# Optimization experiments

Measured on AMD Instinct MI355X. Metric: run time of the kernel, lower is better.

The kernel has to match this reference:

```python
import jax, jax.numpy as jnp
import numpy as np

USER = 100000
ITEM = 50000
N = USER + ITEM
LATDIM = 64
IMG_DIM = 1024
E_ADJ = 3_000_000
E_IMG = 1_000_000
GNN_LAYERS = 2
RIS_LAMBDA = 1.0
EPS = 1e-12


def spmm(rows, cols, vals, x):
    # sparse [N,N] @ dense [N,D] via gather + segment-sum
    return jax.ops.segment_sum(vals[:, None] * x[cols], rows, num_segments=N)


def setup_inputs() -> dict:
    key = jax.random.key(0)
    ks = jax.random.split(key, 10)
    return {
        "adj_rows": jax.random.randint(ks[0], (E_ADJ,), 0, N, dtype=jnp.int32),
        "adj_cols": jax.random.randint(ks[1], (E_ADJ,), 0, N, dtype=jnp.int32),
        "adj_vals": jax.random.uniform(ks[2], (E_ADJ,), dtype=jnp.float32),
        "img_rows": jax.random.randint(ks[3], (E_IMG,), 0, N, dtype=jnp.int32),
        "img_cols": jax.random.randint(ks[4], (E_IMG,), 0, N, dtype=jnp.int32),
        "img_vals": jax.random.uniform(ks[5], (E_IMG,), dtype=jnp.float32),
        "image_embedding": jax.random.normal(ks[6], (ITEM, IMG_DIM), dtype=jnp.float32),
        "uEmbeds": jax.random.normal(ks[7], (USER, LATDIM), dtype=jnp.float32) * 0.01,
        "iEmbeds": jax.random.normal(ks[8], (ITEM, LATDIM), dtype=jnp.float32) * 0.01,
        "W_trans": jax.random.normal(ks[9], (IMG_DIM, LATDIM), dtype=jnp.float32) * (1.0 / np.sqrt(IMG_DIM)),
        "b_trans": jnp.zeros((LATDIM,), dtype=jnp.float32),
    }


def reference(adj_rows, adj_cols, adj_vals, img_rows, img_cols, img_vals,
              image_embedding, uEmbeds, iEmbeds, W_trans, b_trans):
    # trans == 1: Linear projection of image features
    image_feats = image_embedding @ W_trans + b_trans  # [ITEM, LATDIM]

    # image_adj @ concat(u, i)
    embeds_img_adj = spmm(img_rows, img_cols, img_vals, jnp.concatenate([uEmbeds, iEmbeds], axis=0))

    # F.normalize(image_feats) along dim=1 (L2, eps=1e-12)
    nrm = jnp.linalg.norm(image_feats, axis=1, keepdims=True)
    feats_n = image_feats / jnp.maximum(nrm, EPS)

    embeds_image = spmm(adj_rows, adj_cols, adj_vals, jnp.concatenate([uEmbeds, feats_n], axis=0))
    embeds_image_ = spmm(adj_rows, adj_cols, adj_vals,
                         jnp.concatenate([embeds_image[:USER], iEmbeds], axis=0))
    embeds_image = embeds_image + embeds_image_ + RIS_LAMBDA * embeds_img_adj

    # stacked GCN layers with sum over all layer outputs (including input)
    acc = embeds_image
    cur = embeds_image
    for _ in range(GNN_LAYERS):
        cur = spmm(adj_rows, adj_cols, adj_vals, cur)
        acc = acc + cur

    return acc[:USER], acc[USER:]
```

## Files before the change

kernel.cpp:

```cpp
#include <hip/hip_runtime.h>
#include <hip/hip_fp16.h>

#define USER_N 100000
#define ITEM_N 50000
#define NN (USER_N + ITEM_N)
#define D 64
#define IMGD 1024
#define LDP 68

#define BUCKET_BITS 10
#define BROWS (1 << BUCKET_BITS)
#define NBUCK ((NN + BROWS - 1) >> BUCKET_BITS)
#define CHUNK 4096

typedef _Float16 v4h __attribute__((ext_vector_type(4)));
typedef _Float16 v8h __attribute__((ext_vector_type(8)));
typedef float v4f __attribute__((ext_vector_type(4)));

__global__ __launch_bounds__(256) void wt_prep(
    const float* __restrict__ W, _Float16* __restrict__ Wt16)
{
    const int id = blockIdx.x * 256 + threadIdx.x;
    if (id >= D * IMGD) return;
    const int c = id >> 10;
    const int k = id & 1023;
    Wt16[id] = (_Float16)W[(size_t)k * D + c];
}

#define GAS2 68
__global__ __launch_bounds__(256) void gemm_mfma2(
    const float* __restrict__ A, const _Float16* __restrict__ Wt16,
    const float* __restrict__ b, float* __restrict__ C)
{
    __shared__ _Float16 Af[2][32][GAS2];
    const int t = threadIdx.x;
    const int w = t >> 6;
    const int lane = t & 63;
    const int l16 = lane & 15;
    const int g = lane >> 4;
    const int row0 = blockIdx.x * 32;
    const int wr = (w >> 1) * 16;
    const int wc = (w & 1) * 32;

    v4f acc[2] = {};

    const int lrow0 = t >> 4;
    const int lrow1 = lrow0 + 16;
    const int lk = (t & 15) * 4;
    const int ga0 = row0 + lrow0, ga1 = row0 + lrow1;

    {
        float4 v0 = make_float4(0.f, 0.f, 0.f, 0.f), v1 = v0;
        if (ga0 < ITEM_N) v0 = *reinterpret_cast<const float4*>(&A[(size_t)ga0 * IMGD + lk]);
        if (ga1 < ITEM_N) v1 = *reinterpret_cast<const float4*>(&A[(size_t)ga1 * IMGD + lk]);
        v4h h0, h1;
        h0[0] = (_Float16)v0.x; h0[1] = (_Float16)v0.y; h0[2] = (_Float16)v0.z; h0[3] = (_Float16)v0.w;
        h1[0] = (_Float16)v1.x; h1[1] = (_Float16)v1.y; h1[2] = (_Float16)v1.z; h1[3] = (_Float16)v1.w;
        *reinterpret_cast<v4h*>(&Af[0][lrow0][lk]) = h0;
        *reinterpret_cast<v4h*>(&Af[0][lrow1][lk]) = h1;
    }
    __syncthreads();

    for (int k0 = 0; k0 < IMGD; k0 += 64) {
        const int cur = (k0 >> 6) & 1;
        const bool has_next = (k0 + 64) < IMGD;
        float4 n0 = make_float4(0.f, 0.f, 0.f, 0.f), n1 = n0;
        if (has_next) {
            if (ga0 < ITEM_N) n0 = *reinterpret_cast<const float4*>(&A[(size_t)ga0 * IMGD + k0 + 64 + lk]);
            if (ga1 < ITEM_N) n1 = *reinterpret_cast<const float4*>(&A[(size_t)ga1 * IMGD + k0 + 64 + lk]);
        }
#pragma unroll
        for (int s = 0; s < 2; s++) {
            const int kb = s * 32;
            union { v8h v; v4h h[2]; } af;
            af.h[0] = *reinterpret_cast<const v4h*>(&Af[cur][wr + l16][kb + g * 4]);
            af.h[1] = *reinterpret_cast<const v4h*>(&Af[cur][wr + l16][kb + 16 + g * 4]);
#pragma unroll
            for (int n = 0; n < 2; n++) {
                const _Float16* wp = Wt16 + (size_t)(wc + n * 16 + l16) * IMGD + k0 + kb + g * 4;
                union { v8h v; v4h h[2]; } bf;
                bf.h[0] = *reinterpret_cast<const v4h*>(wp);
                bf.h[1] = *reinterpret_cast<const v4h*>(wp + 16);
                acc[n] = __builtin_amdgcn_mfma_f32_16x16x32_f16(af.v, bf.v, acc[n], 0, 0, 0);
            }
        }
        if (has_next) {
            __syncthreads();
            v4h h0, h1;
            h0[0] = (_Float16)n0.x; h0[1] = (_Float16)n0.y; h0[2] = (_Float16)n0.z; h0[3] = (_Float16)n0.w;
            h1[0] = (_Float16)n1.x; h1[1] = (_Float16)n1.y; h1[2] = (_Float16)n1.z; h1[3] = (_Float16)n1.w;
            *reinterpret_cast<v4h*>(&Af[cur ^ 1][lrow0][lk]) = h0;
            *reinterpret_cast<v4h*>(&Af[cur ^ 1][lrow1][lk]) = h1;
            __syncthreads();
        }
    }
#pragma unroll
    for (int n = 0; n < 2; n++) {
        const int col = wc + n * 16 + l16;
        const float bias = b[col];
#pragma unroll
        for (int r = 0; r < 4; r++) {
            const int grow = row0 + wr + g * 4 + r;
            if (grow < ITEM_N)
                C[(size_t)grow * D + col] = acc[n][r] + bias;
        }
    }
}

__global__ __launch_bounds__(256) void gemm_feats32(
    const float* __restrict__ A, const float* __restrict__ W,
    const float* __restrict__ b, float* __restrict__ C)
{
    __shared__ float As[32][LDP];
    __shared__ float Ws[64][LDP];
    const int row0 = blockIdx.x * 32;
    const int t = threadIdx.x;
    const int tx = t & 15, ty = t >> 4;
    float acc[2][4] = {};

    const int lr = t >> 4;
    const int lk = (t & 15) * 4;

    for (int k0 = 0; k0 < IMGD; k0 += 64) {
#pragma unroll
        for (int i = 0; i < 2; i++) {
            const int r = lr + i * 16;
            const int grow = row0 + r;
            float4 v = make_float4(0.f, 0.f, 0.f, 0.f);
            if (grow < ITEM_N)
                v = *reinterpret_cast<const float4*>(&A[(size_t)grow * IMGD + k0 + lk]);
            *reinterpret_cast<float4*>(&As[r][lk]) = v;
        }
#pragma unroll
        for (int i = 0; i < 4; i++) {
            const int kr = lr + i * 16;
            float4 v = *reinterpret_cast<const float4*>(&W[(size_t)(k0 + kr) * D + lk]);
            *reinterpret_cast<float4*>(&Ws[kr][lk]) = v;
        }
        __syncthreads();
#pragma unroll
        for (int kb = 0; kb < 16; kb++) {
            float a_[2][4], w_[4][4];
#pragma unroll
            for (int i = 0; i < 2; i++) {
                const float4 v = *reinterpret_cast<const float4*>(&As[ty * 2 + i][kb * 4]);
                a_[i][0] = v.x; a_[i][1] = v.y; a_[i][2] = v.z; a_[i][3] = v.w;
            }
#pragma unroll
            for (int j = 0; j < 4; j++) {
                const float4 v = *reinterpret_cast<const float4*>(&Ws[kb * 4 + j][tx * 4]);
                w_[j][0] = v.x; w_[j][1] = v.y; w_[j][2] = v.z; w_[j][3] = v.w;
            }
#pragma unroll
            for (int j = 0; j < 4; j++)
#pragma unroll
                for (int i = 0; i < 2; i++)
#pragma unroll
                    for (int c = 0; c < 4; c++)
                        acc[i][c] += a_[i][j] * w_[j][c];
        }
        __syncthreads();
    }
    const float4 bias = *reinterpret_cast<const float4*>(&b[tx * 4]);
#pragma unroll
    for (int i = 0; i < 2; i++) {
        const int grow = row0 + ty * 2 + i;
        if (grow < ITEM_N) {
            float4 v;
            v.x = acc[i][0] + bias.x;
            v.y = acc[i][1] + bias.y;
            v.z = acc[i][2] + bias.z;
            v.w = acc[i][3] + bias.w;
            *reinterpret_cast<float4*>(&C[(size_t)grow * D + tx * 4]) = v;
        }
    }
}

__global__ __launch_bounds__(256) void rownorm_h(
    const float* __restrict__ X, __half* __restrict__ Y, int nrows)
{
    const int gid = blockIdx.x * blockDim.x + threadIdx.x;
    const int row = gid >> 6;
    const int lane = threadIdx.x & 63;
    if (row >= nrows) return;
    float v = X[(size_t)row * D + lane];
    float s = v * v;
#pragma unroll
    for (int o = 32; o > 0; o >>= 1) s += __shfl_xor(s, o, 64);
    const float scale = 1.0f / fmaxf(sqrtf(s), 1e-12f);
    Y[(size_t)row * D + lane] = __float2half(v * scale);
}

__global__ __launch_bounds__(256) void rownorm(float* __restrict__ X, int nrows)
{
    const int gid = blockIdx.x * blockDim.x + threadIdx.x;
    const int row = gid >> 6;
    const int lane = threadIdx.x & 63;
    if (row >= nrows) return;
    float v = X[(size_t)row * D + lane];
    float s = v * v;
#pragma unroll
    for (int o = 32; o > 0; o >>= 1) s += __shfl_xor(s, o, 64);
    const float scale = 1.0f / fmaxf(sqrtf(s), 1e-12f);
    X[(size_t)row * D + lane] = v * scale;
}

__global__ __launch_bounds__(256) void cvt_f2h(
    const float* __restrict__ s, __half* __restrict__ d, int n4)
{
    const int i = blockIdx.x * blockDim.x + threadIdx.x;
    if (i >= n4) return;
    const float4 v = reinterpret_cast<const float4*>(s)[i];
    __half2* d2 = reinterpret_cast<__half2*>(d);
    d2[2 * i]     = __floats2half2_rn(v.x, v.y);
    d2[2 * i + 1] = __floats2half2_rn(v.z, v.w);
}

__global__ __launch_bounds__(256) void bucket_count(
    const int* __restrict__ rows, int nnz, int nb, int* __restrict__ histT)
{
    __shared__ int cnt[NBUCK];
    for (int i = threadIdx.x; i < NBUCK; i += 256) cnt[i] = 0;
    __syncthreads();
    const int e0 = blockIdx.x * CHUNK;
    const int e1 = min(e0 + CHUNK, nnz);
    for (int e = e0 + threadIdx.x; e < e1; e += 256)
        atomicAdd(&cnt[rows[e] >> BUCKET_BITS], 1);
    __syncthreads();
    for (int b = threadIdx.x; b < NBUCK; b += 256)
        histT[b * nb + blockIdx.x] = cnt[b];
}

__global__ __launch_bounds__(1024) void scanA(
    const int* __restrict__ cnt, int* __restrict__ excl,
    int* __restrict__ blocksums, int n)
{
    const int t = threadIdx.x;
    const int gid = blockIdx.x * 1024 + t;
    const int lane = t & 63, wid = t >> 6;
    int v = (gid < n) ? cnt[gid] : 0;
    int x = v;
#pragma unroll
    for (int o = 1; o < 64; o <<= 1) {
        int y = __shfl_up(x, o, 64);
        if (lane >= o) x += y;
    }
    __shared__ int ws[16];
    __shared__ int wo[16];
    if (lane == 63) ws[wid] = x;
    __syncthreads();
    if (t < 16) {
        int s = ws[t];
        int xx = s;
#pragma unroll
        for (int o = 1; o < 16; o <<= 1) {
            int y = __shfl_up(xx, o, 16);
            if (t >= o) xx += y;
        }
        wo[t] = xx - s;
        if (t == 15) blocksums[blockIdx.x] = xx;
    }
    __syncthreads();
    if (gid < n) excl[gid] = x - v + wo[wid];
}

__global__ __launch_bounds__(1024) void scanB(int* __restrict__ bs, int nb)
{
    const int t = threadIdx.x;
    const int lane = t & 63, wid = t >> 6;
    int v = (t < nb) ? bs[t] : 0;
    int x = v;
#pragma unroll
    for (int o = 1; o < 64; o <<= 1) {
        int y = __shfl_up(x, o, 64);
        if (lane >= o) x += y;
    }
    __shared__ int ws[16];
    __shared__ int wo[16];
    if (lane == 63) ws[wid] = x;
    __syncthreads();
    if (t < 16) {
        int s = ws[t];
        int xx = s;
#pragma unroll
        for (int o = 1; o < 16; o <<= 1) {
            int y = __shfl_up(xx, o, 16);
            if (t >= o) xx += y;
        }
        wo[t] = xx - s;
    }
    __syncthreads();
    if (t < nb) bs[t] = x - v + wo[wid];
}

__global__ __launch_bounds__(256) void scan_apply(
    int* __restrict__ excl, const int* __restrict__ bo, int n)
{
    const int gid = blockIdx.x * blockDim.x + threadIdx.x;
    if (gid < n) excl[gid] += bo[gid >> 10];
}

__global__ __launch_bounds__(256) void bucket_place(
    const int* __restrict__ rows, const int* __restrict__ cols,
    const float* __restrict__ vals, int nnz, int nb,
    const int* __restrict__ offsT, uint2* __restrict__ rec)
{
    __shared__ int cur[NBUCK];
    for (int b = threadIdx.x; b < NBUCK; b += 256)
        cur[b] = offsT[b * nb + blockIdx.x];
    __syncthreads();
    const int e0 = blockIdx.x * CHUNK;
    const int e1 = min(e0 + CHUNK, nnz);
    for (int e = e0 + threadIdx.x; e < e1; e += 256) {
        const int r = rows[e];
        const int b = r >> BUCKET_BITS;
        const int pos = atomicAdd(&cur[b], 1);
        rec[pos] = make_uint2(((unsigned)cols[e] << BUCKET_BITS) |
                                  (unsigned)(r & (BROWS - 1)),
                              __float_as_uint(vals[e]));
    }
}

__global__ __launch_bounds__(1024) void bucket_finalize(
    const uint2* __restrict__ rec, int nnz, int nb,
    const int* __restrict__ offsT, int* __restrict__ rp,
    int2* __restrict__ ev)
{
    const int b = blockIdx.x;
    const int t = threadIdx.x;
    const int rlo = b << BUCKET_BITS;
    const int segs = offsT[b * nb];
    const int sege = (b + 1 < NBUCK) ? offsT[(b + 1) * nb] : nnz;

    __shared__ int cnt[BROWS];
    __shared__ int cur[BROWS];
    cnt[t] = 0;
    __syncthreads();
    for (int i = segs + t; i < sege; i += 1024)
        atomicAdd(&cnt[rec[i].x & (BROWS - 1)], 1);
    __syncthreads();

    const int lane = t & 63, wid = t >> 6;
    const int v = cnt[t];
    int x = v;
#pragma unroll
    for (int o = 1; o < 64; o <<= 1) {
        int y = __shfl_up(x, o, 64);
        if (lane >= o) x += y;
    }
    __shared__ int wsum[16];
    __shared__ int woff[16];
    if (lane == 63) wsum[wid] = x;
    __syncthreads();
    if (t < 16) {
        int s = wsum[t];
        int xx = s;
#pragma unroll
        for (int o = 1; o < 16; o <<= 1) {
            int y = __shfl_up(xx, o, 16);
            if (t >= o) xx += y;
        }
        woff[t] = xx - s;
    }
    __syncthreads();
    const int start = segs + (x - v + woff[wid]);

    if (rlo + t < NN) rp[rlo + t] = start;
    if (b == NBUCK - 1 && t == 0) rp[NN] = nnz;
    cur[t] = start;
    __syncthreads();

    for (int i = segs + t; i < sege; i += 1024) {
        const uint2 R = rec[i];
        const int rl = (int)(R.x & (BROWS - 1));
        const int c = (int)(R.x >> BUCKET_BITS);
        const int pos = atomicAdd(&cur[rl], 1);
        ev[pos] = make_int2(c, (int)R.y);
    }
}

__global__ __launch_bounds__(256) void spmm_h8(
    const int* __restrict__ rp, const int2* __restrict__ ev,
    const __half* __restrict__ src,
    float* __restrict__ out32, __half* __restrict__ out16, int limit16,
    const float* __restrict__ add1, const float* __restrict__ add2)
{
    const int wid = (blockIdx.x * 256 + threadIdx.x) >> 6;
    const int lane = threadIdx.x & 63;
    const int sub = lane >> 3;
    const int l8 = lane & 7;
    const int rowbase = wid * 8;
    if (rowbase >= NN) return;
    const int row = rowbase + sub;

    int v = 0;
    if (lane <= 8 && rowbase + lane <= NN) v = rp[rowbase + lane];
    const int s = __shfl(v, sub, 64);
    const int e = __shfl(v, sub + 1, 64);

    const __half* srcl = src + l8 * 8;
    float acc[8] = {};

    union cvt4 { uint4 u; __half2 h[4]; };
    int i = s;
    for (; i + 3 < e; i += 4) {
        const int2 E0 = ev[i], E1 = ev[i + 1], E2 = ev[i + 2], E3 = ev[i + 3];
        cvt4 g0, g1, g2, g3;
        g0.u = *reinterpret_cast<const uint4*>(srcl + (size_t)E0.x * D);
        g1.u = *reinterpret_cast<const uint4*>(srcl + (size_t)E1.x * D);
        g2.u = *reinterpret_cast<const uint4*>(srcl + (size_t)E2.x * D);
        g3.u = *reinterpret_cast<const uint4*>(srcl + (size_t)E3.x * D);
#pragma unroll
        for (int k = 0; k < 4; k++) {
            const cvt4& g = k == 0 ? g0 : k == 1 ? g1 : k == 2 ? g2 : g3;
            const float w = __int_as_float(k == 0 ? E0.y : k == 1 ? E1.y
                                           : k == 2 ? E2.y : E3.y);
#pragma unroll
            for (int j = 0; j < 4; j++) {
                const float2 f = __half22float2(g.h[j]);
                acc[2 * j]     += w * f.x;
                acc[2 * j + 1] += w * f.y;
            }
        }
    }
    for (; i < e; i++) {
        const int2 E0 = ev[i];
        cvt4 g;
        g.u = *reinterpret_cast<const uint4*>(srcl + (size_t)E0.x * D);
        const float w = __int_as_float(E0.y);
#pragma unroll
        for (int j = 0; j < 4; j++) {
            const float2 f = __half22float2(g.h[j]);
            acc[2 * j]     += w * f.x;
            acc[2 * j + 1] += w * f.y;
        }
    }

    if (row >= NN) return;
    const size_t idx = (size_t)row * D + l8 * 8;
#pragma unroll
    for (int h = 0; h < 2; h++) {
        if (add1) {
            const float4 a = *reinterpret_cast<const float4*>(&add1[idx + h * 4]);
            acc[4 * h] += a.x; acc[4 * h + 1] += a.y;
            acc[4 * h + 2] += a.z; acc[4 * h + 3] += a.w;
        }
        if (add2) {
            const float4 a = *reinterpret_cast<const float4*>(&add2[idx + h * 4]);
            acc[4 * h] += a.x; acc[4 * h + 1] += a.y;
            acc[4 * h + 2] += a.z; acc[4 * h + 3] += a.w;
        }
        float4 o;
        o.x = acc[4 * h]; o.y = acc[4 * h + 1];
        o.z = acc[4 * h + 2]; o.w = acc[4 * h + 3];
        *reinterpret_cast<float4*>(&out32[idx + h * 4]) = o;
    }
    if (row < limit16) {
        cvt4 o16;
#pragma unroll
        for (int j = 0; j < 4; j++)
            o16.h[j] = __floats2half2_rn(acc[2 * j], acc[2 * j + 1]);
        *reinterpret_cast<uint4*>(&out16[idx]) = o16.u;
    }
}

__global__ __launch_bounds__(256) void spmm_csr(
    const int* __restrict__ rp, const int2* __restrict__ ev,
    const float* __restrict__ srcU, const float* __restrict__ srcI,
    float* __restrict__ out,
    const float* __restrict__ add1, const float* __restrict__ add2)
{
    const int gid = blockIdx.x * blockDim.x + threadIdx.x;
    const int row = gid >> 6;
    const int lane = threadIdx.x & 63;
    if (row >= NN) return;
    const int s = rp[row], e = rp[row + 1];
    float acc = 0.f;
    int i = s;
    for (; i + 3 < e; i += 4) {
        const int2 e0 = ev[i], e1 = ev[i + 1], e2 = ev[i + 2], e3 = ev[i + 3];
        const float* p0 = (e0.x < USER_N) ? (srcU + (size_t)e0.x * D)
                                          : (srcI + (size_t)(e0.x - USER_N) * D);
        const float* p1 = (e1.x < USER_N) ? (srcU + (size_t)e1.x * D)
                                          : (srcI + (size_t)(e1.x - USER_N) * D);
        const float* p2 = (e2.x < USER_N) ? (srcU + (size_t)e2.x * D)
                                          : (srcI + (size_t)(e2.x - USER_N) * D);
        const float* p3 = (e3.x < USER_N) ? (srcU + (size_t)e3.x * D)
                                          : (srcI + (size_t)(e3.x - USER_N) * D);
        acc += __int_as_float(e0.y) * p0[lane];
        acc += __int_as_float(e1.y) * p1[lane];
        acc += __int_as_float(e2.y) * p2[lane];
        acc += __int_as_float(e3.y) * p3[lane];
    }
    for (; i < e; i++) {
        const int2 e0 = ev[i];
        const float* p0 = (e0.x < USER_N) ? (srcU + (size_t)e0.x * D)
                                          : (srcI + (size_t)(e0.x - USER_N) * D);
        acc += __int_as_float(e0.y) * p0[lane];
    }
    const size_t idx = (size_t)row * D + lane;
    if (add1) acc += add1[idx];
    if (add2) acc += add2[idx];
    out[idx] = acc;
}

extern "C" void kernel_launch(void* const* d_in, const int* in_sizes, int n_in,
                              void* d_out, int out_size, void* d_ws, size_t ws_size,
                              hipStream_t stream)
{
    const int*   adj_rows = (const int*)d_in[0];
    const int*   adj_cols = (const int*)d_in[1];
    const float* adj_vals = (const float*)d_in[2];
    const int*   img_rows = (const int*)d_in[3];
    const int*   img_cols = (const int*)d_in[4];
    const float* img_vals = (const float*)d_in[5];
    const float* img_emb  = (const float*)d_in[6];
    const float* uEmb     = (const float*)d_in[7];
    const float* iEmb     = (const float*)d_in[8];
    const float* Wt       = (const float*)d_in[9];
    const float* bt       = (const float*)d_in[10];
    float* out = (float*)d_out;

    const int e_adj = in_sizes[0];
    const int e_img = in_sizes[3];
    const int e_max = e_adj > e_img ? e_adj : e_img;
    const int NB_adj = (e_adj + CHUNK - 1) / CHUNK;
    const int NB_img = (e_img + CHUNK - 1) / CHUNK;
    const int NB_max = NB_adj > NB_img ? NB_adj : NB_img;

    const size_t ndbytes = (size_t)NN * D * sizeof(float);
    const size_t nhbytes = (size_t)NN * D * sizeof(__half);

    size_t off = 0;
    auto carve = [&](size_t bytes) { size_t p = off; off += (bytes + 255) & ~(size_t)255; return p; };
    char* base = (char*)d_ws;
    const size_t o_featsN = carve((size_t)ITEM_N * D * sizeof(float));
    const size_t o_bufA   = carve(ndbytes);
    const size_t o_bufB   = carve(ndbytes);
    const size_t o_rpAdj  = carve((NN + 1) * sizeof(int));
    const size_t o_rpImg  = carve((NN + 1) * sizeof(int));
    const size_t o_bsums  = carve(1024 * sizeof(int));
    const size_t o_histT  = carve((size_t)NBUCK * NB_max * sizeof(int));
    const size_t o_rec    = carve((size_t)e_max * sizeof(uint2) > nhbytes
                                      ? (size_t)e_max * sizeof(uint2) : nhbytes);
    const size_t o_evAdj  = carve((size_t)e_adj * sizeof(int2));
    const size_t need_base = off;
    const size_t o_evImg  = carve((size_t)e_img * sizeof(int2) > nhbytes
                                      ? (size_t)e_img * sizeof(int2) : nhbytes);
    const size_t o_x0     = carve(nhbytes);
    const size_t o_wt16   = carve((size_t)D * IMGD * sizeof(_Float16));
    const size_t need_h = off;

    if (ws_size < need_base) return;
    const bool use_h = (ws_size >= need_h);

    float* featsN = (float*)(base + o_featsN);
    float* bufA   = (float*)(base + o_bufA);
    float* bufB   = (float*)(base + o_bufB);
    int* rpAdj    = (int*)(base + o_rpAdj);
    int* rpImg    = (int*)(base + o_rpImg);
    int* bsums    = (int*)(base + o_bsums);
    int* histT    = (int*)(base + o_histT);
    uint2* rec    = (uint2*)(base + o_rec);
    int2* evAdj   = (int2*)(base + o_evAdj);
    int2* evImg   = (int2*)(base + o_evImg);
    __half* xC    = (__half*)(base + o_rec);
    __half* xB    = (__half*)(base + o_evImg);
    __half* x0    = (__half*)(base + o_x0);
    _Float16* wt16 = (_Float16*)(base + o_wt16);

    {
        const int n = NBUCK * NB_adj;
        const int nsb = (n + 1023) / 1024;
        bucket_count<<<NB_adj, 256, 0, stream>>>(adj_rows, e_adj, NB_adj, histT);
        scanA<<<nsb, 1024, 0, stream>>>(histT, histT, bsums, n);
        scanB<<<1, 1024, 0, stream>>>(bsums, nsb);
        scan_apply<<<(n + 255) / 256, 256, 0, stream>>>(histT, bsums, n);
        bucket_place<<<NB_adj, 256, 0, stream>>>(
            adj_rows, adj_cols, adj_vals, e_adj, NB_adj, histT, rec);
        bucket_finalize<<<NBUCK, 1024, 0, stream>>>(
            rec, e_adj, NB_adj, histT, rpAdj, evAdj);
    }
    {
        const int n = NBUCK * NB_img;
        const int nsb = (n + 1023) / 1024;
        bucket_count<<<NB_img, 256, 0, stream>>>(img_rows, e_img, NB_img, histT);
        scanA<<<nsb, 1024, 0, stream>>>(histT, histT, bsums, n);
        scanB<<<1, 1024, 0, stream>>>(bsums, nsb);
        scan_apply<<<(n + 255) / 256, 256, 0, stream>>>(histT, bsums, n);
        bucket_place<<<NB_img, 256, 0, stream>>>(
            img_rows, img_cols, img_vals, e_img, NB_img, histT, rec);
        bucket_finalize<<<NBUCK, 1024, 0, stream>>>(
            rec, e_img, NB_img, histT, rpImg, evImg);
    }

    const int SPMM8_GRID = (NN + 31) / 32;
    const int SPMM_GRID = (NN * 64 + 255) / 256;
    const int RN_GRID = (ITEM_N * 64 + 255) / 256;

    if (use_h) {
        __half* x0I = x0 + (size_t)USER_N * D;
        __half* xBI = xB + (size_t)USER_N * D;

        cvt_f2h<<<(USER_N * D / 4 + 255) / 256, 256, 0, stream>>>(
            uEmb, x0, USER_N * D / 4);
        cvt_f2h<<<(ITEM_N * D / 4 + 255) / 256, 256, 0, stream>>>(
            iEmb, x0I, ITEM_N * D / 4);

        spmm_h8<<<SPMM8_GRID, 256, 0, stream>>>(
            rpImg, evImg, x0, bufA, nullptr, 0, nullptr, nullptr);

        wt_prep<<<(D * IMGD + 255) / 256, 256, 0, stream>>>(Wt, wt16);
        gemm_mfma2<<<(ITEM_N + 31) / 32, 256, 0, stream>>>(img_emb, wt16, bt, featsN);
        rownorm_h<<<RN_GRID, 256, 0, stream>>>(featsN, x0I, ITEM_N);

        cvt_f2h<<<(ITEM_N * D / 4 + 255) / 256, 256, 0, stream>>>(
            iEmb, xBI, ITEM_N * D / 4);

        spmm_h8<<<SPMM8_GRID, 256, 0, stream>>>(
            rpAdj, evAdj, x0, bufB, xB, USER_N, nullptr, nullptr);

        spmm_h8<<<SPMM8_GRID, 256, 0, stream>>>(
            rpAdj, evAdj, xB, bufA, xC, NN, bufB, bufA);

        spmm_h8<<<SPMM8_GRID, 256, 0, stream>>>(
            rpAdj, evAdj, xC, bufB, x0, NN, nullptr, nullptr);

        spmm_h8<<<SPMM8_GRID, 256, 0, stream>>>(
            rpAdj, evAdj, x0, out, nullptr, 0, bufA, bufB);
    } else {
        gemm_feats32<<<(ITEM_N + 31) / 32, 256, 0, stream>>>(img_emb, Wt, bt, featsN);
        rownorm<<<RN_GRID, 256, 0, stream>>>(featsN, ITEM_N);

        spmm_csr<<<SPMM_GRID, 256, 0, stream>>>(
            rpImg, evImg, uEmb, iEmb, bufA, nullptr, nullptr);
        spmm_csr<<<SPMM_GRID, 256, 0, stream>>>(
            rpAdj, evAdj, uEmb, featsN, bufB, nullptr, nullptr);
        spmm_csr<<<SPMM_GRID, 256, 0, stream>>>(
            rpAdj, evAdj, bufB, iEmb, bufA, bufB, bufA);
        spmm_csr<<<SPMM_GRID, 256, 0, stream>>>(
            rpAdj, evAdj, bufA, bufA + (size_t)USER_N * D, bufB, nullptr, nullptr);
        spmm_csr<<<SPMM_GRID, 256, 0, stream>>>(
            rpAdj, evAdj, bufB, bufB + (size_t)USER_N * D, out, bufA, bufB);
    }
}
```

Baseline: 598.7 us.

## Replace shared-memory GEMM with per-wave register-direct MFMA over 16 rows

The image-projection GEMM now gives each wave 16 full rows and all 64 output columns. A operands are loaded straight from global memory into registers and converted to fp16 there, replacing the double-buffered LDS tile and its block-wide barriers. The aim is to remove LDS traffic and synchronisation while keeping each A element read once; the trade-off is that every wave reads the full W panel from global/L2 instead of sharing it, and there are more registers per thread.

Measured after the change: 622.7 us. +4.0%, slower.

```diff
diff --git a/kernel.cpp b/kernel.cpp
--- a/kernel.cpp
+++ b/kernel.cpp
@@ -27,80 +27,84 @@
     Wt16[id] = (_Float16)W[(size_t)k * D + c];
 }
 
-#define GAS2 68
-__global__ __launch_bounds__(256) void gemm_mfma2(
+__global__ __launch_bounds__(256) void gemm_mfma3(
     const float* __restrict__ A, const _Float16* __restrict__ Wt16,
     const float* __restrict__ b, float* __restrict__ C)
 {
-    __shared__ _Float16 Af[2][32][GAS2];
     const int t = threadIdx.x;
-    const int w = t >> 6;
+    const int gwave = (blockIdx.x * 256 + t) >> 6;
     const int lane = t & 63;
     const int l16 = lane & 15;
     const int g = lane >> 4;
-    const int row0 = blockIdx.x * 32;
-    const int wr = (w >> 1) * 16;
-    const int wc = (w & 1) * 32;
-
-    v4f acc[2] = {};
-
-    const int lrow0 = t >> 4;
-    const int lrow1 = lrow0 + 16;
-    const int lk = (t & 15) * 4;
-    const int ga0 = row0 + lrow0, ga1 = row0 + lrow1;
-
-    {
-        float4 v0 = make_float4(0.f, 0.f, 0.f, 0.f), v1 = v0;
-        if (ga0 < ITEM_N) v0 = *reinterpret_cast<const float4*>(&A[(size_t)ga0 * IMGD + lk]);
-        if (ga1 < ITEM_N) v1 = *reinterpret_cast<const float4*>(&A[(size_t)ga1 * IMGD + lk]);
-        v4h h0, h1;
-        h0[0] = (_Float16)v0.x; h0[1] = (_Float16)v0.y; h0[2] = (_Float16)v0.z; h0[3] = (_Float16)v0.w;
-        h1[0] = (_Float16)v1.x; h1[1] = (_Float16)v1.y; h1[2] = (_Float16)v1.z; h1[3] = (_Float16)v1.w;
-        *reinterpret_cast<v4h*>(&Af[0][lrow0][lk]) = h0;
-        *reinterpret_cast<v4h*>(&Af[0][lrow1][lk]) = h1;
-    }
-    __syncthreads();
+    const int row0 = gwave * 16;
+    if (row0 >= ITEM_N) return;
+    const int arow = row0 + l16;
+    const bool rv = arow < ITEM_N;
+    const float* ap = A + (size_t)arow * IMGD + g * 4;
+    const _Float16* wbase = Wt16 + (size_t)l16 * IMGD + g * 4;
+
+    v4f acc[4] = {};
+
+    float4 a[4];
+#pragma unroll
+    for (int j = 0; j < 4; j++) a[j] = make_float4(0.f, 0.f, 0.f, 0.f);
+    if (rv) {
+#pragma unroll
+        for (int j = 0; j < 4; j++)
+            a[j] = *reinterpret_cast<const float4*>(ap + j * 16);
+    }
 
     for (int k0 = 0; k0 < IMGD; k0 += 64) {
-        const int cur = (k0 >> 6) & 1;
-        const bool has_next = (k0 + 64) < IMGD;
-        float4 n0 = make_float4(0.f, 0.f, 0.f, 0.f), n1 = n0;
-        if (has_next) {
-            if (ga0 < ITEM_N) n0 = *reinterpret_cast<const float4*>(&A[(size_t)ga0 * IMGD + k0 + 64 + lk]);
-            if (ga1 < ITEM_N) n1 = *reinterpret_cast<const float4*>(&A[(size_t)ga1 * IMGD + k0 + 64 + lk]);
-        }
-#pragma unroll
-        for (int s = 0; s < 2; s++) {
-            const int kb = s * 32;
-            union { v8h v; v4h h[2]; } af;
-            af.h[0] = *reinterpret_cast<const v4h*>(&Af[cur][wr + l16][kb + g * 4]);
-            af.h[1] = *reinterpret_cast<const v4h*>(&Af[cur][wr + l16][kb + 16 + g * 4]);
-#pragma unroll
-            for (int n = 0; n < 2; n++) {
-                const _Float16* wp = Wt16 + (size_t)(wc + n * 16 + l16) * IMGD + k0 + kb + g * 4;
-                union { v8h v; v4h h[2]; } bf;
-                bf.h[0] = *reinterpret_cast<const v4h*>(wp);
-                bf.h[1] = *reinterpret_cast<const v4h*>(wp + 16);
-                acc[n] = __builtin_amdgcn_mfma_f32_16x16x32_f16(af.v, bf.v, acc[n], 0, 0, 0);
-            }
-        }
-        if (has_next) {
-            __syncthreads();
-            v4h h0, h1;
-            h0[0] = (_Float16)n0.x; h0[1] = (_Float16)n0.y; h0[2] = (_Float16)n0.z; h0[3] = (_Float16)n0.w;
-            h1[0] = (_Float16)n1.x; h1[1] = (_Float16)n1.y; h1[2] = (_Float16)n1.z; h1[3] = (_Float16)n1.w;
-            *reinterpret_cast<v4h*>(&Af[cur ^ 1][lrow0][lk]) = h0;
-            *reinterpret_cast<v4h*>(&Af[cur ^ 1][lrow1][lk]) = h1;
-            __syncthreads();
-        }
-    }
-#pragma unroll
-    for (int n = 0; n < 2; n++) {
-        const int col = wc + n * 16 + l16;
+        float4 na[4];
+#pragma unroll
+        for (int j = 0; j < 4; j++) na[j] = make_float4(0.f, 0.f, 0.f, 0.f);
+        if (rv && (k0 + 64) < IMGD) {
+#pragma unroll
+            for (int j = 0; j < 4; j++)
+                na[j] = *reinterpret_cast<const float4*>(ap + k0 + 64 + j * 16);
+        }
+        union { v8h v; v4h h[2]; } af0, af1;
+        {
+            v4h h;
+            h[0] = (_Float16)a[0].x; h[1] = (_Float16)a[0].y;
+            h[2] = (_Float16)a[0].z; h[3] = (_Float16)a[0].w;
+            af0.h[0] = h;
+            h[0] = (_Float16)a[1].x; h[1] = (_Float16)a[1].y;
+            h[2] = (_Float16)a[1].z; h[3] = (_Float16)a[1].w;
+            af0.h[1] = h;
+            h[0] = (_Float16)a[2].x; h[1] = (_Float16)a[2].y;
+            h[2] = (_Float16)a[2].z; h[3] = (_Float16)a[2].w;
+            af1.h[0] = h;
+            h[0] = (_Float16)a[3].x; h[1] = (_Float16)a[3].y;
+            h[2] = (_Float16)a[3].z; h[3] = (_Float16)a[3].w;
+            af1.h[1] = h;
+        }
+#pragma unroll
+        for (int n = 0; n < 4; n++) {
+            const _Float16* wp = wbase + (size_t)(n * 16) * IMGD + k0;
+            union { v8h v; v4h h[2]; } bf;
+            bf.h[0] = *reinterpret_cast<const v4h*>(wp);
+            bf.h[1] = *reinterpret_cast<const v4h*>(wp + 16);
+            acc[n] = __builtin_amdgcn_mfma_f32_16x16x32_f16(af0.v, bf.v, acc[n], 0, 0, 0);
+        }
+#pragma unroll
+        for (int n = 0; n < 4; n++) {
+            const _Float16* wp = wbase + (size_t)(n * 16) * IMGD + k0 + 32;
+            union { v8h v; v4h h[2]; } bf;
+            bf.h[0] = *reinterpret_cast<const v4h*>(wp);
+            bf.h[1] = *reinterpret_cast<const v4h*>(wp + 16);
+            acc[n] = __builtin_amdgcn_mfma_f32_16x16x32_f16(af1.v, bf.v, acc[n], 0, 0, 0);
+        }
+#pragma unroll
+        for (int j = 0; j < 4; j++) a[j] = na[j];
+    }
+#pragma unroll
+    for (int n = 0; n < 4; n++) {
+        const int col = n * 16 + l16;
         const float bias = b[col];
 #pragma unroll
         for (int r = 0; r < 4; r++) {
-            const int grow = row0 + wr + g * 4 + r;
+            const int grow = row0 + g * 4 + r;
             if (grow < ITEM_N)
                 C[(size_t)grow * D + col] = acc[n][r] + bias;
         }
@@ -597,6 +601,7 @@
     const int SPMM8_GRID = (NN + 31) / 32;
     const int SPMM_GRID = (NN * 64 + 255) / 256;
     const int RN_GRID = (ITEM_N * 64 + 255) / 256;
+    const int GEMM3_GRID = ((ITEM_N + 15) / 16 + 3) / 4;
 
     if (use_h) {
         __half* x0I = x0 + (size_t)USER_N * D;
@@ -611,7 +616,7 @@
             rpImg, evImg, x0, bufA, nullptr, 0, nullptr, nullptr);
 
         wt_prep<<<(D * IMGD + 255) / 256, 256, 0, stream>>>(Wt, wt16);
-        gemm_mfma2<<<(ITEM_N + 31) / 32, 256, 0, stream>>>(img_emb, wt16, bt, featsN);
+        gemm_mfma3<<<GEMM3_GRID, 256, 0, stream>>>(img_emb, wt16, bt, featsN);
         rownorm_h<<<RN_GRID, 256, 0, stream>>>(featsN, x0I, ITEM_N);
 
         cvt_f2h<<<(ITEM_N * D / 4 + 255) / 256, 256, 0, stream>>>(
```
